# Kernel optimization log

Hardware: AMD Instinct MI355X
Metric: run time of the kernel (lower is better)

The kernel has to match this reference:

```python
import jax, jax.numpy as jnp
import numpy as np

NEG_SLOPE = 0.2  # PyG GATConv default LeakyReLU slope


def gat_layer(x, edge_index, W, att_src, att_dst, bias, concat, num_nodes):
    """PyG GATConv (add_self_loops=False, dropout=0, bias=True).
    x: [N, in], W: [in, H*C], att_src/att_dst: [H, C], bias: [H*C] or [C].
    """
    H, C = att_src.shape
    h = (x @ W).reshape(num_nodes, H, C)                      # [N, H, C]
    src, dst = edge_index[0], edge_index[1]                   # messages src -> dst
    a_src = jnp.sum(h * att_src[None], axis=-1)               # [N, H]
    a_dst = jnp.sum(h * att_dst[None], axis=-1)               # [N, H]
    e = jax.nn.leaky_relu(a_src[src] + a_dst[dst], NEG_SLOPE)  # [E, H]
    # segment softmax over edges sharing the same dst node
    e_max = jax.ops.segment_max(e, dst, num_segments=num_nodes)
    e_max = jnp.where(jnp.isfinite(e_max), e_max, 0.0)
    ex = jnp.exp(e - e_max[dst])
    denom = jax.ops.segment_sum(ex, dst, num_segments=num_nodes)
    alpha = ex / (denom[dst] + 1e-16)                          # [E, H]
    msg = h[src] * alpha[:, :, None]                           # [E, H, C]
    out = jax.ops.segment_sum(msg, dst, num_segments=num_nodes)  # [N, H, C]
    out = out.reshape(num_nodes, H * C) if concat else out.mean(axis=1)
    return out + bias


def setup_inputs() -> dict:
    key = jax.random.key(0)
    ks = jax.random.split(key, 12)
    NU, NI, D, H, C = 40000, 40000, 64, 2, 64
    N = NU + NI
    E = 1_280_000
    B = 8192
    s = 0.05
    return {
        "Gu": jax.random.normal(ks[0], (NU, D), jnp.float32) * s,
        "Gi": jax.random.normal(ks[1], (NI, D), jnp.float32) * s,
        "W0": jax.random.normal(ks[2], (D, H * C), jnp.float32) * s,
        "att_src0": jax.random.normal(ks[3], (H, C), jnp.float32) * s,
        "att_dst0": jax.random.normal(ks[4], (H, C), jnp.float32) * s,
        "b0": jnp.zeros((H * C,), jnp.float32),
        "W1": jax.random.normal(ks[5], (H * C, H * C), jnp.float32) * s,
        "att_src1": jax.random.normal(ks[6], (H, C), jnp.float32) * s,
        "att_dst1": jax.random.normal(ks[7], (H, C), jnp.float32) * s,
        "b1": jnp.zeros((C,), jnp.float32),
        "edge_index": jax.random.randint(ks[8], (2, E), 0, N, jnp.int32),
        "user_idx": jax.random.randint(ks[9], (B,), 0, NU, jnp.int32),
        "item_idx": jax.random.randint(ks[10], (B,), 0, NI, jnp.int32),
    }


def reference(Gu, Gi, W0, att_src0, att_dst0, b0, W1, att_src1, att_dst1, b1,
              edge_index, user_idx, item_idx):
    num_users = Gu.shape[0]
    x = jnp.concatenate([Gu, Gi], axis=0)
    N = x.shape[0]
    # layer 0: concat=True, layer 1 (final): concat=False (mean over heads)
    x = gat_layer(x, edge_index, W0, att_src0, att_dst0, b0, True, N)
    x = gat_layer(x, edge_index, W1, att_src1, att_dst1, b1, False, N)
    gu, gi = x[:num_users], x[num_users:]
    # forward(): rowwise dot product of user/item embeddings
    xui = jnp.sum(gu[user_idx] * gi[item_idx], axis=1)
    return xui
```

## Files before the change

### kernel.cpp

```cpp
#include <hip/hip_runtime.h>
#include <hip/hip_fp16.h>
#include <math.h>

#define N_NODES   80000
#define NU_NODES  40000
#define E_EDGES   1280000
#define B_PAIRS   8192
#define NEG_SLOPE 0.2f
#define NBUCK     313
#define SCHUNK    2048

typedef _Float16 half8 __attribute__((ext_vector_type(8)));
typedef float    f32x4 __attribute__((ext_vector_type(4)));


__global__ void hist_kernel(const int* __restrict__ dst, int* __restrict__ counts, int E) {
    int e = blockIdx.x * 256 + threadIdx.x;
    if (e < E) atomicAdd(&counts[dst[e]], 1);
}

__global__ __launch_bounds__(256) void scan256_kernel(const int* __restrict__ counts,
                                                      int* __restrict__ row_ptr,
                                                      int* __restrict__ bsums) {
    __shared__ int tmp[256];
    int t = threadIdx.x;
    int gid = (blockIdx.x << 8) + t;
    int v = (gid < N_NODES) ? counts[gid] : 0;
    tmp[t] = v;
    __syncthreads();
    for (int off = 1; off < 256; off <<= 1) {
        int x = (t >= off) ? tmp[t - off] : 0;
        __syncthreads();
        tmp[t] += x;
        __syncthreads();
    }
    if (gid < N_NODES) row_ptr[gid + 1] = tmp[t];
    if (t == 255) bsums[blockIdx.x] = tmp[255];
}

__global__ __launch_bounds__(512) void topscan_kernel(const int* __restrict__ bsums,
                                                      int* __restrict__ bucket_ptr,
                                                      int* __restrict__ gfill) {
    __shared__ int tmp[512];
    int t = threadIdx.x;
    int v = (t < NBUCK) ? bsums[t] : 0;
    tmp[t] = v;
    __syncthreads();
    for (int off = 1; off < 512; off <<= 1) {
        int x = (t >= off) ? tmp[t - off] : 0;
        __syncthreads();
        tmp[t] += x;
        __syncthreads();
    }
    int excl = tmp[t] - v;
    if (t < NBUCK) {
        bucket_ptr[t] = excl;
        gfill[t]      = excl;
        if (t == NBUCK - 1) bucket_ptr[NBUCK] = excl + v;
    }
}

__global__ void fixup_kernel(int* row_ptr, const int* __restrict__ bucket_ptr) {
    int gid = blockIdx.x * 256 + threadIdx.x;
    if (gid < N_NODES) row_ptr[gid + 1] += bucket_ptr[gid >> 8];
    if (gid == 0) row_ptr[0] = 0;
}


__global__ __launch_bounds__(512) void bscatter_kernel(const int* __restrict__ src,
                                                       const int* __restrict__ dst,
                                                       int* __restrict__ gfill,
                                                       unsigned long long* __restrict__ pk,
                                                       int E) {
    __shared__ int histL[NBUCK];
    __shared__ int baseL[NBUCK];
    __shared__ int rankL[NBUCK];
    for (int i = threadIdx.x; i < NBUCK; i += 512) { histL[i] = 0; rankL[i] = 0; }
    __syncthreads();
    int base = blockIdx.x * SCHUNK;
#pragma unroll
    for (int r = 0; r < SCHUNK / 512; ++r) {
        int e = base + r * 512 + threadIdx.x;
        if (e < E) atomicAdd(&histL[dst[e] >> 8], 1);
    }
    __syncthreads();
    for (int i = threadIdx.x; i < NBUCK; i += 512)
        baseL[i] = histL[i] ? atomicAdd(&gfill[i], histL[i]) : 0;
    __syncthreads();
#pragma unroll
    for (int r = 0; r < SCHUNK / 512; ++r) {
        int e = base + r * 512 + threadIdx.x;
        if (e < E) {
            int d = dst[e];
            int b = d >> 8;
            int rk = atomicAdd(&rankL[b], 1);
            pk[baseL[b] + rk] = ((unsigned long long)(unsigned)d << 32) | (unsigned)src[e];
        }
    }
}

__global__ __launch_bounds__(256) void escatter_kernel(const unsigned long long* __restrict__ pk,
                                                       const int* __restrict__ bucket_ptr,
                                                       const int* __restrict__ row_ptr,
                                                       int* __restrict__ src_sorted) {
    __shared__ int fillL[256];
    __shared__ int rpL[256];
    int b = blockIdx.x;
    int node0 = b << 8;
    int nn = N_NODES - node0; if (nn > 256) nn = 256;
    fillL[threadIdx.x] = 0;
    rpL[threadIdx.x]   = (threadIdx.x < nn) ? row_ptr[node0 + threadIdx.x] : 0;
    __syncthreads();
    int s = bucket_ptr[b], e = bucket_ptr[b + 1];
    for (int k = s + threadIdx.x; k < e; k += 256) {
        unsigned long long p = pk[k];
        int lo = (int)(p >> 32) & 255;
        int pos = atomicAdd(&fillL[lo], 1);
        src_sorted[rpL[lo] + pos] = (int)(unsigned)p;
    }
}


template <int K, bool AF32>
__global__ __launch_bounds__(256) void gemm_mfma(const void* __restrict__ A0v,
                                                 const void* __restrict__ A1v, int split,
                                                 const float* __restrict__ W,
                                                 const float* __restrict__ attS,
                                                 const float* __restrict__ attD,
                                                 __half* __restrict__ hh,
                                                 float* __restrict__ a_s,
                                                 float* __restrict__ a_d) {
    constexpr int BSTR   = K + 8;
    constexpr int BSM_SZ = 128 * BSTR * 2;
    constexpr int EPI_SZ = 128 * 136 * 2;
    constexpr int ATT_OFF = (10240 + BSM_SZ > EPI_SZ) ? (10240 + BSM_SZ) : EPI_SZ;
    __shared__ __align__(16) char lds[ATT_OFF + 1024];
    _Float16* Asm  = (_Float16*)lds;
    _Float16* Bsm  = (_Float16*)(lds + 10240);
    _Float16* epi  = (_Float16*)lds;
    float*    attL = (float*)(lds + ATT_OFF);

    const int tid    = threadIdx.x;
    const int w      = tid >> 6;
    const int l      = tid & 63;
    const int l15    = l & 15;
    const int g      = l >> 4;
    const int blkrow = blockIdx.x * 128;

    attL[tid] = (tid < 128) ? attS[tid] : attD[tid - 128];

    for (int idx = tid; idx < K * 32; idx += 256) {
        int k = idx >> 5, c4 = idx & 31;
        float4 wv = *(const float4*)&W[(size_t)k * 128 + c4 * 4];
        Bsm[(c4 * 4 + 0) * BSTR + k] = (_Float16)wv.x;
        Bsm[(c4 * 4 + 1) * BSTR + k] = (_Float16)wv.y;
        Bsm[(c4 * 4 + 2) * BSTR + k] = (_Float16)wv.z;
        Bsm[(c4 * 4 + 3) * BSTR + k] = (_Float16)wv.w;
    }

    const void* rowp[2];
#pragma unroll
    for (int p = 0; p < 2; ++p) {
        int idx = tid + p * 256;
        int row = idx >> 2;
        int grow = blkrow + row;
        if (AF32) {
            const float* A0 = (const float*)A0v;
            const float* A1 = (const float*)A1v;
            rowp[p] = (grow < split) ? (const void*)(A0 + (size_t)grow * K)
                                     : (const void*)(A1 + (size_t)(grow - split) * K);
        } else {
            rowp[p] = (const void*)((const _Float16*)A0v + (size_t)grow * K);
        }
    }

    auto stageA = [&](int c) {
#pragma unroll
        for (int p = 0; p < 2; ++p) {
            int idx = tid + p * 256;
            int row = idx >> 2, kq = idx & 3;
            half8 hv;
            if (AF32) {
                const float* ap = (const float*)rowp[p];
                float4 v0 = *(const float4*)&ap[c * 32 + kq * 8];
                float4 v1 = *(const float4*)&ap[c * 32 + kq * 8 + 4];
                hv[0] = (_Float16)v0.x; hv[1] = (_Float16)v0.y;
                hv[2] = (_Float16)v0.z; hv[3] = (_Float16)v0.w;
                hv[4] = (_Float16)v1.x; hv[5] = (_Float16)v1.y;
                hv[6] = (_Float16)v1.z; hv[7] = (_Float16)v1.w;
            } else {
                const _Float16* ap = (const _Float16*)rowp[p];
                hv = *(const half8*)&ap[c * 32 + kq * 8];
            }
            *(half8*)&Asm[row * 40 + kq * 8] = hv;
        }
    };

    f32x4 acc[2][8];
#pragma unroll
    for (int rt = 0; rt < 2; ++rt)
#pragma unroll
        for (int ct = 0; ct < 8; ++ct) acc[rt][ct] = (f32x4){0.f, 0.f, 0.f, 0.f};

    constexpr int CH = K / 32;
    stageA(0);
    __syncthreads();
#pragma unroll
    for (int c = 0; c < CH; ++c) {
        half8 a0 = *(const half8*)&Asm[(w * 32 + l15) * 40 + g * 8];
        half8 a1 = *(const half8*)&Asm[(w * 32 + 16 + l15) * 40 + g * 8];
#pragma unroll
        for (int ct = 0; ct < 8; ++ct) {
            half8 b = *(const half8*)&Bsm[(ct * 16 + l15) * BSTR + c * 32 + g * 8];
            acc[0][ct] = __builtin_amdgcn_mfma_f32_16x16x32_f16(a0, b, acc[0][ct], 0, 0, 0);
            acc[1][ct] = __builtin_amdgcn_mfma_f32_16x16x32_f16(a1, b, acc[1][ct], 0, 0, 0);
        }
        __syncthreads();
        if (c + 1 < CH) {
            stageA(c + 1);
            __syncthreads();
        }
    }

#pragma unroll
    for (int rt = 0; rt < 2; ++rt)
#pragma unroll
        for (int reg = 0; reg < 4; ++reg) {
            float s0 = 0.f, s1 = 0.f, d0 = 0.f, d1 = 0.f;
#pragma unroll
            for (int ct = 0; ct < 4; ++ct) {
                float v = acc[rt][ct][reg];
                s0 = fmaf(v, attL[ct * 16 + l15], s0);
                d0 = fmaf(v, attL[128 + ct * 16 + l15], d0);
            }
#pragma unroll
            for (int ct = 4; ct < 8; ++ct) {
                float v = acc[rt][ct][reg];
                s1 = fmaf(v, attL[ct * 16 + l15], s1);
                d1 = fmaf(v, attL[128 + ct * 16 + l15], d1);
            }
#pragma unroll
            for (int o = 1; o < 16; o <<= 1) {
                s0 += __shfl_xor(s0, o); s1 += __shfl_xor(s1, o);
                d0 += __shfl_xor(d0, o); d1 += __shfl_xor(d1, o);
            }
            if (l15 == 0) {
                int row = blkrow + w * 32 + rt * 16 + g * 4 + reg;
                *(float2*)&a_s[row * 2] = make_float2(s0, s1);
                *(float2*)&a_d[row * 2] = make_float2(d0, d1);
            }
        }

#pragma unroll
    for (int rt = 0; rt < 2; ++rt)
#pragma unroll
        for (int ct = 0; ct < 8; ++ct)
#pragma unroll
            for (int reg = 0; reg < 4; ++reg)
                epi[(w * 32 + rt * 16 + g * 4 + reg) * 136 + ct * 16 + l15] =
                    (_Float16)acc[rt][ct][reg];
    __syncthreads();
#pragma unroll
    for (int p = 0; p < 8; ++p) {
        int idx = tid + p * 256;
        int row = idx >> 4, c8 = idx & 15;
        *(half8*)&hh[(size_t)(blkrow + row) * 128 + c8 * 8] =
            *(const half8*)&epi[row * 136 + c8 * 8];
    }
}


#define RLI(x, j) __builtin_amdgcn_readlane((x), (j))
#define RLF(x, j) __int_as_float(__builtin_amdgcn_readlane(__float_as_int(x), (j)))

template <bool CONCAT>
__global__ __launch_bounds__(256) void gat_agg_kernel(const __half* __restrict__ hh,
        const int* __restrict__ row_ptr, const int* __restrict__ src_sorted,
        const float* __restrict__ a_s, const float* __restrict__ a_d,
        const float* __restrict__ bias, void* __restrict__ outv) {
    __shared__ int   s_idx[4][64];
    __shared__ float s_w[4][64][2];
    int wid   = threadIdx.x >> 6;
    int lane  = threadIdx.x & 63;
    int dnode = blockIdx.x * 4 + wid;
    if (dnode >= N_NODES) return;
    int start = row_ptr[dnode], end = row_ptr[dnode + 1];
    int deg = end - start;
    float2 ad = *(const float2*)(a_d + dnode * 2);
    int hh_head = lane >> 5;
    float2 acc = {0.f, 0.f};
    float den0 = 0.f, den1 = 0.f;
    const __half2* h2 = (const __half2*)hh;

    if (deg <= 64) {
        float w0v = 0.f, w1v = 0.f;
        int s = 0;
        if (lane < deg) {
            s = src_sorted[start + lane];
            float2 as = *(const float2*)(a_s + s * 2);
            float v0 = as.x + ad.x; v0 = v0 > 0.f ? v0 : NEG_SLOPE * v0;
            float v1 = as.y + ad.y; v1 = v1 > 0.f ? v1 : NEG_SLOPE * v1;
            w0v = __expf(v0); w1v = __expf(v1);
        }
        den0 = w0v; den1 = w1v;
        for (int o = 32; o; o >>= 1) {
            den0 += __shfl_xor(den0, o);
            den1 += __shfl_xor(den1, o);
        }
        int j = 0;
#pragma unroll 1
        for (; j + 4 <= deg; j += 4) {
            int si0 = RLI(s, j + 0), si1 = RLI(s, j + 1);
            int si2 = RLI(s, j + 2), si3 = RLI(s, j + 3);
            float wa = hh_head ? RLF(w1v, j + 0) : RLF(w0v, j + 0);
            float wb = hh_head ? RLF(w1v, j + 1) : RLF(w0v, j + 1);
            float wc = hh_head ? RLF(w1v, j + 2) : RLF(w0v, j + 2);
            float wd = hh_head ? RLF(w1v, j + 3) : RLF(w0v, j + 3);
            float2 q0 = __half22float2(h2[(size_t)si0 * 64 + lane]);
            float2 q1 = __half22float2(h2[(size_t)si1 * 64 + lane]);
            float2 q2 = __half22float2(h2[(size_t)si2 * 64 + lane]);
            float2 q3 = __half22float2(h2[(size_t)si3 * 64 + lane]);
            acc.x = fmaf(wa, q0.x, acc.x); acc.y = fmaf(wa, q0.y, acc.y);
            acc.x = fmaf(wb, q1.x, acc.x); acc.y = fmaf(wb, q1.y, acc.y);
            acc.x = fmaf(wc, q2.x, acc.x); acc.y = fmaf(wc, q2.y, acc.y);
            acc.x = fmaf(wd, q3.x, acc.x); acc.y = fmaf(wd, q3.y, acc.y);
        }
        for (; j < deg; ++j) {
            int   si = RLI(s, j);
            float we = hh_head ? RLF(w1v, j) : RLF(w0v, j);
            float2 v = __half22float2(h2[(size_t)si * 64 + lane]);
            acc.x = fmaf(we, v.x, acc.x);
            acc.y = fmaf(we, v.y, acc.y);
        }
    } else {
        for (int c0 = start; c0 < end; c0 += 64) {
            int len = min(64, end - c0);
            if (lane < len) {
                int s = src_sorted[c0 + lane];
                float2 as = *(const float2*)(a_s + s * 2);
                float v0 = as.x + ad.x; v0 = v0 > 0.f ? v0 : NEG_SLOPE * v0;
                float v1 = as.y + ad.y; v1 = v1 > 0.f ? v1 : NEG_SLOPE * v1;
                float w0 = __expf(v0), w1 = __expf(v1);
                den0 += w0; den1 += w1;
                s_idx[wid][lane] = s;
                s_w[wid][lane][0] = w0;
                s_w[wid][lane][1] = w1;
            }
            for (int j = 0; j < len; ++j) {
                int  si = s_idx[wid][j];
                float w = s_w[wid][j][hh_head];
                float2 v = __half22float2(h2[(size_t)si * 64 + lane]);
                acc.x = fmaf(w, v.x, acc.x);
                acc.y = fmaf(w, v.y, acc.y);
            }
        }
        for (int o = 32; o; o >>= 1) {
            den0 += __shfl_xor(den0, o);
            den1 += __shfl_xor(den1, o);
        }
    }

    float inv = 1.f / ((hh_head ? den1 : den0) + 1e-16f);
    float2 r = {acc.x * inv, acc.y * inv};

    if (CONCAT) {
        __half* out = (__half*)outv;
        float2 b = *(const float2*)(bias + lane * 2);
        __half2 o2 = __floats2half2_rn(r.x + b.x, r.y + b.y);
        *(__half2*)(out + (size_t)dnode * 128 + lane * 2) = o2;
    } else {
        float* out = (float*)outv;
        float ox = __shfl_xor(r.x, 32);
        float oy = __shfl_xor(r.y, 32);
        if (lane < 32) {
            float2 b = *(const float2*)(bias + lane * 2);
            float2 o2 = {0.5f * (r.x + ox) + b.x, 0.5f * (r.y + oy) + b.y};
            *(float2*)(out + (size_t)dnode * 64 + lane * 2) = o2;
        }
    }
}


__global__ void pair_dot_kernel(const float* __restrict__ emb, const int* __restrict__ ui,
                                const int* __restrict__ ii, float* __restrict__ out, int B) {
    int w    = blockIdx.x * 4 + (threadIdx.x >> 6);
    int lane = threadIdx.x & 63;
    if (w >= B) return;
    float a = emb[(size_t)ui[w] * 64 + lane];
    float b = emb[(size_t)(NU_NODES + ii[w]) * 64 + lane];
    float p = a * b;
    for (int o = 32; o; o >>= 1) p += __shfl_xor(p, o);
    if (lane == 0) out[w] = p;
}

extern "C" void kernel_launch(void* const* d_in, const int* in_sizes, int n_in,
                              void* d_out, int out_size, void* d_ws, size_t ws_size,
                              hipStream_t stream) {
    const float* Gu       = (const float*)d_in[0];
    const float* Gi       = (const float*)d_in[1];
    const float* W0       = (const float*)d_in[2];
    const float* att_src0 = (const float*)d_in[3];
    const float* att_dst0 = (const float*)d_in[4];
    const float* b0       = (const float*)d_in[5];
    const float* W1       = (const float*)d_in[6];
    const float* att_src1 = (const float*)d_in[7];
    const float* att_dst1 = (const float*)d_in[8];
    const float* b1       = (const float*)d_in[9];
    const int* edge_index = (const int*)d_in[10];
    const int* user_idx   = (const int*)d_in[11];
    const int* item_idx   = (const int*)d_in[12];
    float* outp           = (float*)d_out;

    const int N = N_NODES, E = E_EDGES;
    char* wsp = (char*)d_ws;
    auto alloc = [&](size_t bytes) {
        void* p = wsp;
        wsp += (bytes + 255) & ~(size_t)255;
        return p;
    };
    float*  emb = (float*)alloc((size_t)N * 64 * 4);
    __half* hh  = (__half*)alloc((size_t)N * 128 * 2);
    __half* x1h = (__half*)alloc((size_t)N * 128 * 2);
    float*  a_s = (float*)alloc((size_t)N * 2 * 4);
    float*  a_d = (float*)alloc((size_t)N * 2 * 4);
    int* row_ptr    = (int*)alloc((size_t)(N + 1) * 4);
    int* counts     = (int*)alloc((size_t)N * 4);
    int* bsums      = (int*)alloc(512 * 4);
    int* src_sorted = (int*)alloc((size_t)E * 4);
    int* bucket_ptr  = (int*)alloc((NBUCK + 1) * 4);
    int* gfill       = (int*)alloc((NBUCK + 1) * 4);
    unsigned long long* pk = (unsigned long long*)x1h;

    const int* esrc = edge_index;
    const int* edst = edge_index + E;

    hipMemsetAsync(counts, 0, (size_t)N * 4, stream);
    hist_kernel<<<E / 256, 256, 0, stream>>>(edst, counts, E);
    scan256_kernel<<<NBUCK, 256, 0, stream>>>(counts, row_ptr, bsums);
    topscan_kernel<<<1, 512, 0, stream>>>(bsums, bucket_ptr, gfill);
    fixup_kernel<<<NBUCK, 256, 0, stream>>>(row_ptr, bucket_ptr);

    bscatter_kernel<<<(E + SCHUNK - 1) / SCHUNK, 512, 0, stream>>>(esrc, edst, gfill, pk, E);
    escatter_kernel<<<NBUCK, 256, 0, stream>>>(pk, bucket_ptr, row_ptr, src_sorted);

    gemm_mfma<64, true><<<N / 128, 256, 0, stream>>>(Gu, Gi, NU_NODES, W0, att_src0, att_dst0,
                                                     hh, a_s, a_d);
    gat_agg_kernel<true><<<(N + 3) / 4, 256, 0, stream>>>(hh, row_ptr, src_sorted, a_s, a_d,
                                                          b0, x1h);

    gemm_mfma<128, false><<<N / 128, 256, 0, stream>>>(x1h, x1h, N, W1, att_src1, att_dst1,
                                                       hh, a_s, a_d);
    gat_agg_kernel<false><<<(N + 3) / 4, 256, 0, stream>>>(hh, row_ptr, src_sorted, a_s, a_d,
                                                           b1, emb);

    pair_dot_kernel<<<B_PAIRS / 4, 256, 0, stream>>>(emb, user_idx, item_idx, outp, B_PAIRS);
}
```

Measured before the change: 277.5 us.

## Split per-head feature tables and aggregate each head in its own pass

The GEMM epilogue now writes head 0 and head 1 features to separate contiguous fp16 tables, and aggregation runs as two per-head kernels. Each wave processes two edges at a time, one per half-wave, and combines the halves with a cross-half shuffle. Neighbor indices and weights are staged in LDS instead of being read with readlane. The goal is a smaller gather working set per pass, 5 MB per head table instead of 10 MB, for better cache hit rates on random neighbor gathers. The cost is re-reading row_ptr, src_sorted and a_s per head, twice the launches, and a read-modify-write of emb for the mean in the final layer.

```diff
diff --git a/kernel.cpp b/kernel.cpp
--- a/kernel.cpp
+++ b/kernel.cpp
@@ -65,7 +65,6 @@
     if (gid < N_NODES) row_ptr[gid + 1] += bucket_ptr[gid >> 8];
     if (gid == 0) row_ptr[0] = 0;
 }
-
 
 __global__ __launch_bounds__(512) void bscatter_kernel(const int* __restrict__ src,
                                                        const int* __restrict__ dst,
@@ -127,7 +126,8 @@
                                                  const float* __restrict__ W,
                                                  const float* __restrict__ attS,
                                                  const float* __restrict__ attD,
-                                                 __half* __restrict__ hh,
+                                                 __half* __restrict__ h0,
+                                                 __half* __restrict__ h1,
                                                  float* __restrict__ a_s,
                                                  float* __restrict__ a_d) {
     constexpr int BSTR   = K + 8;
@@ -264,118 +264,122 @@
     for (int p = 0; p < 8; ++p) {
         int idx = tid + p * 256;
         int row = idx >> 4, c8 = idx & 15;
-        *(half8*)&hh[(size_t)(blkrow + row) * 128 + c8 * 8] =
-            *(const half8*)&epi[row * 136 + c8 * 8];
-    }
-}
-
-
-#define RLI(x, j) __builtin_amdgcn_readlane((x), (j))
-#define RLF(x, j) __int_as_float(__builtin_amdgcn_readlane(__float_as_int(x), (j)))
-
-template <bool CONCAT>
-__global__ __launch_bounds__(256) void gat_agg_kernel(const __half* __restrict__ hh,
+        half8 v = *(const half8*)&epi[row * 136 + c8 * 8];
+        if (c8 < 8)
+            *(half8*)&h0[(size_t)(blkrow + row) * 64 + c8 * 8] = v;
+        else
+            *(half8*)&h1[(size_t)(blkrow + row) * 64 + (c8 - 8) * 8] = v;
+    }
+}
+
+
+template <int HEAD, bool CONCAT>
+__global__ __launch_bounds__(256) void gat_agg_head(const __half* __restrict__ hhead,
         const int* __restrict__ row_ptr, const int* __restrict__ src_sorted,
         const float* __restrict__ a_s, const float* __restrict__ a_d,
         const float* __restrict__ bias, void* __restrict__ outv) {
     __shared__ int   s_idx[4][64];
-    __shared__ float s_w[4][64][2];
+    __shared__ float s_w[4][64];
     int wid   = threadIdx.x >> 6;
     int lane  = threadIdx.x & 63;
     int dnode = blockIdx.x * 4 + wid;
     if (dnode >= N_NODES) return;
     int start = row_ptr[dnode], end = row_ptr[dnode + 1];
     int deg = end - start;
-    float2 ad = *(const float2*)(a_d + dnode * 2);
-    int hh_head = lane >> 5;
+    float adh = a_d[dnode * 2 + HEAD];
+    float den = 0.f;
+    const __half2* h2 = (const __half2*)hhead;
+    const int e01 = lane >> 5;
+    const int c   = lane & 31;
     float2 acc = {0.f, 0.f};
-    float den0 = 0.f, den1 = 0.f;
-    const __half2* h2 = (const __half2*)hh;
 
     if (deg <= 64) {
-        float w0v = 0.f, w1v = 0.f;
-        int s = 0;
+        float wv = 0.f;
         if (lane < deg) {
-            s = src_sorted[start + lane];
-            float2 as = *(const float2*)(a_s + s * 2);
-            float v0 = as.x + ad.x; v0 = v0 > 0.f ? v0 : NEG_SLOPE * v0;
-            float v1 = as.y + ad.y; v1 = v1 > 0.f ? v1 : NEG_SLOPE * v1;
-            w0v = __expf(v0); w1v = __expf(v1);
-        }
-        den0 = w0v; den1 = w1v;
-        for (int o = 32; o; o >>= 1) {
-            den0 += __shfl_xor(den0, o);
-            den1 += __shfl_xor(den1, o);
-        }
+            int s = src_sorted[start + lane];
+            float v = a_s[s * 2 + HEAD] + adh;
+            v = v > 0.f ? v : NEG_SLOPE * v;
+            wv = __expf(v);
+            s_idx[wid][lane] = s;
+            s_w[wid][lane]   = wv;
+        }
+        den = wv;
+        for (int o = 32; o; o >>= 1) den += __shfl_xor(den, o);
         int j = 0;
 #pragma unroll 1
-        for (; j + 4 <= deg; j += 4) {
-            int si0 = RLI(s, j + 0), si1 = RLI(s, j + 1);
-            int si2 = RLI(s, j + 2), si3 = RLI(s, j + 3);
-            float wa = hh_head ? RLF(w1v, j + 0) : RLF(w0v, j + 0);
-            float wb = hh_head ? RLF(w1v, j + 1) : RLF(w0v, j + 1);
-            float wc = hh_head ? RLF(w1v, j + 2) : RLF(w0v, j + 2);
-            float wd = hh_head ? RLF(w1v, j + 3) : RLF(w0v, j + 3);
-            float2 q0 = __half22float2(h2[(size_t)si0 * 64 + lane]);
-            float2 q1 = __half22float2(h2[(size_t)si1 * 64 + lane]);
-            float2 q2 = __half22float2(h2[(size_t)si2 * 64 + lane]);
-            float2 q3 = __half22float2(h2[(size_t)si3 * 64 + lane]);
-            acc.x = fmaf(wa, q0.x, acc.x); acc.y = fmaf(wa, q0.y, acc.y);
-            acc.x = fmaf(wb, q1.x, acc.x); acc.y = fmaf(wb, q1.y, acc.y);
-            acc.x = fmaf(wc, q2.x, acc.x); acc.y = fmaf(wc, q2.y, acc.y);
-            acc.x = fmaf(wd, q3.x, acc.x); acc.y = fmaf(wd, q3.y, acc.y);
-        }
-        for (; j < deg; ++j) {
-            int   si = RLI(s, j);
-            float we = hh_head ? RLF(w1v, j) : RLF(w0v, j);
-            float2 v = __half22float2(h2[(size_t)si * 64 + lane]);
-            acc.x = fmaf(we, v.x, acc.x);
-            acc.y = fmaf(we, v.y, acc.y);
+        for (; j + 8 <= deg; j += 8) {
+            int j0 = j + e01, j1 = j + 2 + e01, j2 = j + 4 + e01, j3 = j + 6 + e01;
+            int si0 = s_idx[wid][j0], si1 = s_idx[wid][j1];
+            int si2 = s_idx[wid][j2], si3 = s_idx[wid][j3];
+            float w0 = s_w[wid][j0], w1 = s_w[wid][j1];
+            float w2 = s_w[wid][j2], w3 = s_w[wid][j3];
+            float2 q0 = __half22float2(h2[(size_t)si0 * 32 + c]);
+            float2 q1 = __half22float2(h2[(size_t)si1 * 32 + c]);
+            float2 q2 = __half22float2(h2[(size_t)si2 * 32 + c]);
+            float2 q3 = __half22float2(h2[(size_t)si3 * 32 + c]);
+            acc.x = fmaf(w0, q0.x, acc.x); acc.y = fmaf(w0, q0.y, acc.y);
+            acc.x = fmaf(w1, q1.x, acc.x); acc.y = fmaf(w1, q1.y, acc.y);
+            acc.x = fmaf(w2, q2.x, acc.x); acc.y = fmaf(w2, q2.y, acc.y);
+            acc.x = fmaf(w3, q3.x, acc.x); acc.y = fmaf(w3, q3.y, acc.y);
+        }
+        for (; j < deg; j += 2) {
+            int jj = j + e01;
+            bool val = jj < deg;
+            int   si = s_idx[wid][val ? jj : 0];
+            float w  = val ? s_w[wid][jj] : 0.f;
+            float2 q = __half22float2(h2[(size_t)si * 32 + c]);
+            acc.x = fmaf(w, q.x, acc.x);
+            acc.y = fmaf(w, q.y, acc.y);
         }
     } else {
         for (int c0 = start; c0 < end; c0 += 64) {
             int len = min(64, end - c0);
             if (lane < len) {
                 int s = src_sorted[c0 + lane];
-                float2 as = *(const float2*)(a_s + s * 2);
-                float v0 = as.x + ad.x; v0 = v0 > 0.f ? v0 : NEG_SLOPE * v0;
-                float v1 = as.y + ad.y; v1 = v1 > 0.f ? v1 : NEG_SLOPE * v1;
-                float w0 = __expf(v0), w1 = __expf(v1);
-                den0 += w0; den1 += w1;
+                float v = a_s[s * 2 + HEAD] + adh;
+                v = v > 0.f ? v : NEG_SLOPE * v;
+                float wv = __expf(v);
+                den += wv;
                 s_idx[wid][lane] = s;
-                s_w[wid][lane][0] = w0;
-                s_w[wid][lane][1] = w1;
-            }
-            for (int j = 0; j < len; ++j) {
-                int  si = s_idx[wid][j];
-                float w = s_w[wid][j][hh_head];
-                float2 v = __half22float2(h2[(size_t)si * 64 + lane]);
-                acc.x = fmaf(w, v.x, acc.x);
-                acc.y = fmaf(w, v.y, acc.y);
-            }
-        }
-        for (int o = 32; o; o >>= 1) {
-            den0 += __shfl_xor(den0, o);
-            den1 += __shfl_xor(den1, o);
-        }
-    }
-
-    float inv = 1.f / ((hh_head ? den1 : den0) + 1e-16f);
+                s_w[wid][lane]   = wv;
+            }
+            __builtin_amdgcn_wave_barrier();
+            for (int j = 0; j < len; j += 2) {
+                int jj = j + e01;
+                bool val = jj < len;
+                int   si = s_idx[wid][val ? jj : 0];
+                float w  = val ? s_w[wid][jj] : 0.f;
+                float2 q = __half22float2(h2[(size_t)si * 32 + c]);
+                acc.x = fmaf(w, q.x, acc.x);
+                acc.y = fmaf(w, q.y, acc.y);
+            }
+            __builtin_amdgcn_wave_barrier();
+        }
+        for (int o = 32; o; o >>= 1) den += __shfl_xor(den, o);
+    }
+
+    acc.x += __shfl_xor(acc.x, 32);
+    acc.y += __shfl_xor(acc.y, 32);
+    float inv = 1.f / (den + 1e-16f);
     float2 r = {acc.x * inv, acc.y * inv};
 
-    if (CONCAT) {
-        __half* out = (__half*)outv;
-        float2 b = *(const float2*)(bias + lane * 2);
-        __half2 o2 = __floats2half2_rn(r.x + b.x, r.y + b.y);
-        *(__half2*)(out + (size_t)dnode * 128 + lane * 2) = o2;
-    } else {
-        float* out = (float*)outv;
-        float ox = __shfl_xor(r.x, 32);
-        float oy = __shfl_xor(r.y, 32);
-        if (lane < 32) {
-            float2 b = *(const float2*)(bias + lane * 2);
-            float2 o2 = {0.5f * (r.x + ox) + b.x, 0.5f * (r.y + oy) + b.y};
-            *(float2*)(out + (size_t)dnode * 64 + lane * 2) = o2;
+    if (lane < 32) {
+        if (CONCAT) {
+            __half* out = (__half*)outv;
+            float2 b = *(const float2*)(bias + HEAD * 64 + c * 2);
+            *(__half2*)(out + (size_t)dnode * 128 + HEAD * 64 + c * 2) =
+                __floats2half2_rn(r.x + b.x, r.y + b.y);
+        } else {
+            float* out = (float*)outv;
+            if (HEAD == 0) {
+                float2 b = *(const float2*)(bias + c * 2);
+                float2 o2 = {0.5f * r.x + b.x, 0.5f * r.y + b.y};
+                *(float2*)(out + (size_t)dnode * 64 + c * 2) = o2;
+            } else {
+                float2 cur = *(float2*)(out + (size_t)dnode * 64 + c * 2);
+                float2 o2 = {cur.x + 0.5f * r.x, cur.y + 0.5f * r.y};
+                *(float2*)(out + (size_t)dnode * 64 + c * 2) = o2;
+            }
         }
     }
 }
@@ -419,7 +423,8 @@
         return p;
     };
     float*  emb = (float*)alloc((size_t)N * 64 * 4);
-    __half* hh  = (__half*)alloc((size_t)N * 128 * 2);
+    __half* h0  = (__half*)alloc((size_t)N * 64 * 2);
+    __half* h1  = (__half*)alloc((size_t)N * 64 * 2);
     __half* x1h = (__half*)alloc((size_t)N * 128 * 2);
     float*  a_s = (float*)alloc((size_t)N * 2 * 4);
     float*  a_d = (float*)alloc((size_t)N * 2 * 4);
@@ -444,14 +449,18 @@
     escatter_kernel<<<NBUCK, 256, 0, stream>>>(pk, bucket_ptr, row_ptr, src_sorted);
 
     gemm_mfma<64, true><<<N / 128, 256, 0, stream>>>(Gu, Gi, NU_NODES, W0, att_src0, att_dst0,
-                                                     hh, a_s, a_d);
-    gat_agg_kernel<true><<<(N + 3) / 4, 256, 0, stream>>>(hh, row_ptr, src_sorted, a_s, a_d,
-                                                          b0, x1h);
+                                                     h0, h1, a_s, a_d);
+    gat_agg_head<0, true><<<(N + 3) / 4, 256, 0, stream>>>(h0, row_ptr, src_sorted, a_s, a_d,
+                                                           b0, x1h);
+    gat_agg_head<1, true><<<(N + 3) / 4, 256, 0, stream>>>(h1, row_ptr, src_sorted, a_s, a_d,
+                                                           b0, x1h);
 
     gemm_mfma<128, false><<<N / 128, 256, 0, stream>>>(x1h, x1h, N, W1, att_src1, att_dst1,
-                                                       hh, a_s, a_d);
-    gat_agg_kernel<false><<<(N + 3) / 4, 256, 0, stream>>>(hh, row_ptr, src_sorted, a_s, a_d,
-                                                           b1, emb);
+                                                       h0, h1, a_s, a_d);
+    gat_agg_head<0, false><<<(N + 3) / 4, 256, 0, stream>>>(h0, row_ptr, src_sorted, a_s, a_d,
+                                                            b1, emb);
+    gat_agg_head<1, false><<<(N + 3) / 4, 256, 0, stream>>>(h1, row_ptr, src_sorted, a_s, a_d,
+                                                            b1, emb);
 
     pair_dot_kernel<<<B_PAIRS / 4, 256, 0, stream>>>(emb, user_idx, item_idx, outp, B_PAIRS);
 }
```

After: 313.1 us. 1.13x slower.

## Fuse per-node degree counting into bucket scatter and drop global node histogram

Applied to the files above, without the earlier changes.

Replaces the global per-node atomic histogram, two-level scan and fixup kernels with a shared-memory bucket histogram. Per-node counts and exclusive offsets are now computed inside the per-bucket scatter kernel, which writes row_ptr directly. This cuts kernel launches and the heavy contention of global atomics, at the cost of an extra pass over the packed edges per bucket. The low-degree aggregation path also switches from cross-lane readlane broadcasts to LDS staging of indices and weights.

```diff
diff --git a/kernel.cpp b/kernel.cpp
--- a/kernel.cpp
+++ b/kernel.cpp
@@ -14,36 +14,28 @@
 typedef float    f32x4 __attribute__((ext_vector_type(4)));
 
 
-__global__ void hist_kernel(const int* __restrict__ dst, int* __restrict__ counts, int E) {
-    int e = blockIdx.x * 256 + threadIdx.x;
-    if (e < E) atomicAdd(&counts[dst[e]], 1);
-}
-
-__global__ __launch_bounds__(256) void scan256_kernel(const int* __restrict__ counts,
-                                                      int* __restrict__ row_ptr,
-                                                      int* __restrict__ bsums) {
-    __shared__ int tmp[256];
-    int t = threadIdx.x;
-    int gid = (blockIdx.x << 8) + t;
-    int v = (gid < N_NODES) ? counts[gid] : 0;
-    tmp[t] = v;
-    __syncthreads();
-    for (int off = 1; off < 256; off <<= 1) {
-        int x = (t >= off) ? tmp[t - off] : 0;
-        __syncthreads();
-        tmp[t] += x;
-        __syncthreads();
-    }
-    if (gid < N_NODES) row_ptr[gid + 1] = tmp[t];
-    if (t == 255) bsums[blockIdx.x] = tmp[255];
-}
-
-__global__ __launch_bounds__(512) void topscan_kernel(const int* __restrict__ bsums,
+__global__ __launch_bounds__(512) void bhist313_kernel(const int* __restrict__ dst,
+                                                       int* __restrict__ bucketCount, int E) {
+    __shared__ int histL[NBUCK];
+    for (int i = threadIdx.x; i < NBUCK; i += 512) histL[i] = 0;
+    __syncthreads();
+    int base = blockIdx.x * SCHUNK;
+#pragma unroll
+    for (int r = 0; r < SCHUNK / 512; ++r) {
+        int e = base + r * 512 + threadIdx.x;
+        if (e < E) atomicAdd(&histL[dst[e] >> 8], 1);
+    }
+    __syncthreads();
+    for (int i = threadIdx.x; i < NBUCK; i += 512)
+        if (histL[i]) atomicAdd(&bucketCount[i], histL[i]);
+}
+
+__global__ __launch_bounds__(512) void topscan_kernel(const int* __restrict__ bucketCount,
                                                       int* __restrict__ bucket_ptr,
                                                       int* __restrict__ gfill) {
     __shared__ int tmp[512];
     int t = threadIdx.x;
-    int v = (t < NBUCK) ? bsums[t] : 0;
+    int v = (t < NBUCK) ? bucketCount[t] : 0;
     tmp[t] = v;
     __syncthreads();
     for (int off = 1; off < 512; off <<= 1) {
@@ -59,13 +51,6 @@
         if (t == NBUCK - 1) bucket_ptr[NBUCK] = excl + v;
     }
 }
-
-__global__ void fixup_kernel(int* row_ptr, const int* __restrict__ bucket_ptr) {
-    int gid = blockIdx.x * 256 + threadIdx.x;
-    if (gid < N_NODES) row_ptr[gid + 1] += bucket_ptr[gid >> 8];
-    if (gid == 0) row_ptr[0] = 0;
-}
-
 
 __global__ __launch_bounds__(512) void bscatter_kernel(const int* __restrict__ src,
                                                        const int* __restrict__ dst,
@@ -99,23 +84,40 @@
     }
 }
 
-__global__ __launch_bounds__(256) void escatter_kernel(const unsigned long long* __restrict__ pk,
-                                                       const int* __restrict__ bucket_ptr,
-                                                       const int* __restrict__ row_ptr,
-                                                       int* __restrict__ src_sorted) {
-    __shared__ int fillL[256];
+__global__ __launch_bounds__(256) void escatter2_kernel(
+        const unsigned long long* __restrict__ pk, const int* __restrict__ bucket_ptr,
+        int* __restrict__ row_ptr, int* __restrict__ src_sorted) {
+    __shared__ int cntL[256];
+    __shared__ int tmp[256];
     __shared__ int rpL[256];
     int b = blockIdx.x;
+    int t = threadIdx.x;
     int node0 = b << 8;
-    int nn = N_NODES - node0; if (nn > 256) nn = 256;
-    fillL[threadIdx.x] = 0;
-    rpL[threadIdx.x]   = (threadIdx.x < nn) ? row_ptr[node0 + threadIdx.x] : 0;
-    __syncthreads();
     int s = bucket_ptr[b], e = bucket_ptr[b + 1];
-    for (int k = s + threadIdx.x; k < e; k += 256) {
+    cntL[t] = 0;
+    __syncthreads();
+    for (int k = s + t; k < e; k += 256) atomicAdd(&cntL[(int)(pk[k] >> 32) & 255], 1);
+    __syncthreads();
+    int v = cntL[t];
+    tmp[t] = v;
+    __syncthreads();
+    for (int off = 1; off < 256; off <<= 1) {
+        int x = (t >= off) ? tmp[t - off] : 0;
+        __syncthreads();
+        tmp[t] += x;
+        __syncthreads();
+    }
+    int excl = tmp[t] - v;
+    rpL[t] = s + excl;
+    int node = node0 + t;
+    if (node < N_NODES) row_ptr[node] = s + excl;
+    if (b == NBUCK - 1 && t == 0) row_ptr[N_NODES] = e;
+    cntL[t] = 0;
+    __syncthreads();
+    for (int k = s + t; k < e; k += 256) {
         unsigned long long p = pk[k];
         int lo = (int)(p >> 32) & 255;
-        int pos = atomicAdd(&fillL[lo], 1);
+        int pos = atomicAdd(&cntL[lo], 1);
         src_sorted[rpL[lo] + pos] = (int)(unsigned)p;
     }
 }
@@ -270,9 +272,6 @@
 }
 
 
-#define RLI(x, j) __builtin_amdgcn_readlane((x), (j))
-#define RLF(x, j) __int_as_float(__builtin_amdgcn_readlane(__float_as_int(x), (j)))
-
 template <bool CONCAT>
 __global__ __launch_bounds__(256) void gat_agg_kernel(const __half* __restrict__ hh,
         const int* __restrict__ row_ptr, const int* __restrict__ src_sorted,
@@ -293,16 +292,17 @@
     const __half2* h2 = (const __half2*)hh;
 
     if (deg <= 64) {
-        float w0v = 0.f, w1v = 0.f;
-        int s = 0;
         if (lane < deg) {
-            s = src_sorted[start + lane];
+            int s = src_sorted[start + lane];
             float2 as = *(const float2*)(a_s + s * 2);
             float v0 = as.x + ad.x; v0 = v0 > 0.f ? v0 : NEG_SLOPE * v0;
             float v1 = as.y + ad.y; v1 = v1 > 0.f ? v1 : NEG_SLOPE * v1;
-            w0v = __expf(v0); w1v = __expf(v1);
-        }
-        den0 = w0v; den1 = w1v;
+            float w0 = __expf(v0), w1 = __expf(v1);
+            den0 = w0; den1 = w1;
+            s_idx[wid][lane] = s;
+            s_w[wid][lane][0] = w0;
+            s_w[wid][lane][1] = w1;
+        }
         for (int o = 32; o; o >>= 1) {
             den0 += __shfl_xor(den0, o);
             den1 += __shfl_xor(den1, o);
@@ -310,27 +310,25 @@
         int j = 0;
 #pragma unroll 1
         for (; j + 4 <= deg; j += 4) {
-            int si0 = RLI(s, j + 0), si1 = RLI(s, j + 1);
-            int si2 = RLI(s, j + 2), si3 = RLI(s, j + 3);
-            float wa = hh_head ? RLF(w1v, j + 0) : RLF(w0v, j + 0);
-            float wb = hh_head ? RLF(w1v, j + 1) : RLF(w0v, j + 1);
-            float wc = hh_head ? RLF(w1v, j + 2) : RLF(w0v, j + 2);
-            float wd = hh_head ? RLF(w1v, j + 3) : RLF(w0v, j + 3);
+            int   si0 = s_idx[wid][j + 0], si1 = s_idx[wid][j + 1];
+            int   si2 = s_idx[wid][j + 2], si3 = s_idx[wid][j + 3];
+            float w0 = s_w[wid][j + 0][hh_head], w1 = s_w[wid][j + 1][hh_head];
+            float w2 = s_w[wid][j + 2][hh_head], w3 = s_w[wid][j + 3][hh_head];
             float2 q0 = __half22float2(h2[(size_t)si0 * 64 + lane]);
             float2 q1 = __half22float2(h2[(size_t)si1 * 64 + lane]);
             float2 q2 = __half22float2(h2[(size_t)si2 * 64 + lane]);
             float2 q3 = __half22float2(h2[(size_t)si3 * 64 + lane]);
-            acc.x = fmaf(wa, q0.x, acc.x); acc.y = fmaf(wa, q0.y, acc.y);
-            acc.x = fmaf(wb, q1.x, acc.x); acc.y = fmaf(wb, q1.y, acc.y);
-            acc.x = fmaf(wc, q2.x, acc.x); acc.y = fmaf(wc, q2.y, acc.y);
-            acc.x = fmaf(wd, q3.x, acc.x); acc.y = fmaf(wd, q3.y, acc.y);
+            acc.x = fmaf(w0, q0.x, acc.x); acc.y = fmaf(w0, q0.y, acc.y);
+            acc.x = fmaf(w1, q1.x, acc.x); acc.y = fmaf(w1, q1.y, acc.y);
+            acc.x = fmaf(w2, q2.x, acc.x); acc.y = fmaf(w2, q2.y, acc.y);
+            acc.x = fmaf(w3, q3.x, acc.x); acc.y = fmaf(w3, q3.y, acc.y);
         }
         for (; j < deg; ++j) {
-            int   si = RLI(s, j);
-            float we = hh_head ? RLF(w1v, j) : RLF(w0v, j);
+            int  si = s_idx[wid][j];
+            float w = s_w[wid][j][hh_head];
             float2 v = __half22float2(h2[(size_t)si * 64 + lane]);
-            acc.x = fmaf(we, v.x, acc.x);
-            acc.y = fmaf(we, v.y, acc.y);
+            acc.x = fmaf(w, v.x, acc.x);
+            acc.y = fmaf(w, v.y, acc.y);
         }
     } else {
         for (int c0 = start; c0 < end; c0 += 64) {
@@ -423,10 +421,9 @@
     __half* x1h = (__half*)alloc((size_t)N * 128 * 2);
     float*  a_s = (float*)alloc((size_t)N * 2 * 4);
     float*  a_d = (float*)alloc((size_t)N * 2 * 4);
-    int* row_ptr    = (int*)alloc((size_t)(N + 1) * 4);
-    int* counts     = (int*)alloc((size_t)N * 4);
-    int* bsums      = (int*)alloc(512 * 4);
-    int* src_sorted = (int*)alloc((size_t)E * 4);
+    int* row_ptr     = (int*)alloc((size_t)(N + 1) * 4);
+    int* src_sorted  = (int*)alloc((size_t)E * 4);
+    int* bucketCount = (int*)alloc((NBUCK + 1) * 4);
     int* bucket_ptr  = (int*)alloc((NBUCK + 1) * 4);
     int* gfill       = (int*)alloc((NBUCK + 1) * 4);
     unsigned long long* pk = (unsigned long long*)x1h;
@@ -434,14 +431,12 @@
     const int* esrc = edge_index;
     const int* edst = edge_index + E;
 
-    hipMemsetAsync(counts, 0, (size_t)N * 4, stream);
-    hist_kernel<<<E / 256, 256, 0, stream>>>(edst, counts, E);
-    scan256_kernel<<<NBUCK, 256, 0, stream>>>(counts, row_ptr, bsums);
-    topscan_kernel<<<1, 512, 0, stream>>>(bsums, bucket_ptr, gfill);
-    fixup_kernel<<<NBUCK, 256, 0, stream>>>(row_ptr, bucket_ptr);
-
-    bscatter_kernel<<<(E + SCHUNK - 1) / SCHUNK, 512, 0, stream>>>(esrc, edst, gfill, pk, E);
-    escatter_kernel<<<NBUCK, 256, 0, stream>>>(pk, bucket_ptr, row_ptr, src_sorted);
+    hipMemsetAsync(bucketCount, 0, (NBUCK + 1) * 4, stream);
+    int nblk = (E + SCHUNK - 1) / SCHUNK;
+    bhist313_kernel<<<nblk, 512, 0, stream>>>(edst, bucketCount, E);
+    topscan_kernel<<<1, 512, 0, stream>>>(bucketCount, bucket_ptr, gfill);
+    bscatter_kernel<<<nblk, 512, 0, stream>>>(esrc, edst, gfill, pk, E);
+    escatter2_kernel<<<NBUCK, 256, 0, stream>>>(pk, bucket_ptr, row_ptr, src_sorted);
 
     gemm_mfma<64, true><<<N / 128, 256, 0, stream>>>(Gu, Gi, NU_NODES, W0, att_src0, att_dst0,
                                                      hh, a_s, a_d);
```

Result: faster. 224.5 us (-19.1%).
